# Kernel optimization log

Measured on AMD Instinct MI355X. Metric: run time of the kernel, lower is better.

The kernel has to match this reference:

```python
import jax, jax.numpy as jnp
import numpy as np

N = 50000   # nodes
E = 600000  # edges
F = 128     # num_features
H = 128     # hidden_channels
G = 64      # graphs in batch


def setup_inputs() -> dict:
    key = jax.random.key(0)
    ks = jax.random.split(key, 12)
    x = jax.random.normal(ks[0], (N, F), dtype=jnp.float32)
    edge_index = jax.random.randint(ks[1], (2, E), 0, N, dtype=jnp.int64)
    edge_mask = jax.random.randint(ks[2], (E,), 0, 3, dtype=jnp.int64)
    batch = jnp.sort(jax.random.randint(ks[3], (N,), 0, G, dtype=jnp.int64))
    s = 0.05
    W1 = jax.random.normal(ks[4], (F, H), dtype=jnp.float32) * s
    b1 = jnp.zeros((H,), jnp.float32)
    W2 = jax.random.normal(ks[5], (H, H), dtype=jnp.float32) * s
    b2 = jnp.zeros((H,), jnp.float32)
    W3 = jax.random.normal(ks[6], (H, H), dtype=jnp.float32) * s
    b3 = jnp.zeros((H,), jnp.float32)
    Wl = jax.random.normal(ks[7], (H, 1), dtype=jnp.float32) * s
    bl = jnp.zeros((1,), jnp.float32)
    return {"x": x, "edge_index": edge_index, "edge_mask": edge_mask, "batch": batch,
            "W1": W1, "b1": b1, "W2": W2, "b2": b2, "W3": W3, "b3": b3, "Wl": Wl, "bl": bl}


def gcn_conv(x, W, b, src, dst, ew, n):
    """PyG GCNConv: add self-loops, symmetric deg^-1/2 normalization.
    ew is a {0,1} per-edge weight implementing the dynamic edge subset
    (equivalent to edge_index[:, idx] subsetting, since masked edges
    contribute neither to degree nor to aggregation)."""
    h = x @ W                                                # [n, H]
    deg = jax.ops.segment_sum(ew, dst, num_segments=n) + 1.0  # self-loop adds 1
    dinv = jax.lax.rsqrt(deg)                                # deg^-1/2
    norm = ew * dinv[src] * dinv[dst]                        # per-edge coeff
    agg = jax.ops.segment_sum(h[src] * norm[:, None], dst, num_segments=n)
    agg = agg + h * (dinv * dinv)[:, None]                   # self-loop term 1/deg_i
    return agg + b


def reference(x, edge_index, edge_mask, batch, W1, b1, W2, b2, W3, b3, Wl, bl):
    src, dst = edge_index[0], edge_index[1]
    ones = jnp.ones((E,), x.dtype)
    h = jax.nn.relu(gcn_conv(x, W1, b1, src, dst, ones, N))
    m1 = (edge_mask == 1).astype(x.dtype)
    h = jax.nn.relu(gcn_conv(h, W2, b2, src, dst, m1, N))
    m2 = (edge_mask == 2).astype(x.dtype)
    h = gcn_conv(h, W3, b3, src, dst, m2, N)
    # global_mean_pool over batch ids
    sums = jax.ops.segment_sum(h, batch, num_segments=G)        # [G, H]
    cnt = jax.ops.segment_sum(jnp.ones((N,), h.dtype), batch, num_segments=G)
    pooled = sums / jnp.clip(cnt, 1.0)[:, None]
    # dropout(p=0.3) is identity in eval mode
    return pooled @ Wl + bl
```

## Files before the change

### kernel.cpp

```cpp
#include <hip/hip_runtime.h>

#define NN 50000
#define EE 600000
#define HH 128
#define GG 64
#define NPAD 50176
#define NR 196
#define RN 256
#define NSEC3 150528
#define NRT 588
#define EPB 3072
#define SCAP 3584
#define STAGB 7168

typedef __attribute__((ext_vector_type(8))) short short8;
typedef __attribute__((ext_vector_type(4))) float f32x4;
typedef __attribute__((ext_vector_type(4))) unsigned int u32x4;

__device__ __forceinline__ float bf2f(unsigned int u16) {
    union { unsigned int i; float f; } v; v.i = u16 << 16; return v.f;
}
__device__ __forceinline__ unsigned short f2bf(float f) {
    union { float f; unsigned int i; } v; v.f = f;
    unsigned int u = v.i;
    return (unsigned short)((u + 0x7FFFu + ((u >> 16) & 1u)) >> 16);
}

__device__ __forceinline__ short8 cvt8(f32x4 lo, f32x4 hi) {
    short8 r;
    r[0] = (short)f2bf(lo[0]); r[1] = (short)f2bf(lo[1]);
    r[2] = (short)f2bf(lo[2]); r[3] = (short)f2bf(lo[3]);
    r[4] = (short)f2bf(hi[0]); r[5] = (short)f2bf(hi[1]);
    r[6] = (short)f2bf(hi[2]); r[7] = (short)f2bf(hi[3]);
    return r;
}

__global__ __launch_bounds__(256) void k_part(const int* __restrict__ ei, const int* __restrict__ mask,
                                              int* __restrict__ scnt, unsigned int* __restrict__ sbuf) {
    __shared__ int bcnt[256];
    __shared__ int bcur[256];
    __shared__ int gbase[256];
    int t = threadIdx.x;
    int e0 = blockIdx.x * EPB;
    unsigned int pk[12]; int bin[12];
    bcnt[t] = 0; bcur[t] = 0;
    __syncthreads();
    #pragma unroll
    for (int j = 0; j < 12; j++) {
        int e = e0 + j * 256 + t;
        if (e < EE) {
            int s = ei[e];
            int d = ei[EE + e];
            int m = mask[e];
            pk[j] = (unsigned int)s | ((unsigned int)(d & 255) << 16) | ((unsigned int)m << 24);
            bin[j] = d >> 8;
            atomicAdd(&bcnt[bin[j]], 1);
        } else bin[j] = -1;
    }
    __syncthreads();
    int v = bcnt[t];
    gbase[t] = (v > 0) ? atomicAdd(&scnt[t], v) : 0;
    __syncthreads();
    #pragma unroll
    for (int j = 0; j < 12; j++) {
        if (bin[j] >= 0) {
            int b = bin[j];
            int pos = gbase[b] + atomicAdd(&bcur[b], 1);
            if (pos < SCAP) sbuf[(size_t)b * SCAP + pos] = pk[j];
        }
    }
}

__global__ __launch_bounds__(256) void k_cnt(const int* __restrict__ scnt,
                                             const unsigned int* __restrict__ sbuf,
                                             int* __restrict__ deg, float* __restrict__ dinv,
                                             int* __restrict__ rtot) {
    __shared__ int l0[RN], l1[RN], l2[RN];
    __shared__ int red[12];
    int t = threadIdx.x, lane = t & 63, w = t >> 6;
    int rng = blockIdx.x;
    l0[t] = 0; l1[t] = 0; l2[t] = 0;
    __syncthreads();
    int cnt = scnt[rng]; if (cnt > SCAP) cnt = SCAP;
    const unsigned int* sb = sbuf + (size_t)rng * SCAP;
    for (int i = t; i < cnt; i += 256) {
        unsigned int p = sb[i];
        int dl = (int)((p >> 16) & 255u);
        int m = (int)(p >> 24);
        atomicAdd(&l0[dl], 1);
        if (m == 1) atomicAdd(&l1[dl], 1);
        else if (m == 2) atomicAdd(&l2[dl], 1);
    }
    __syncthreads();
    int node = rng * RN + t;
    int a = l0[t], b = l1[t], c = l2[t];
    deg[node] = a;
    deg[NPAD + node] = b;
    deg[2 * NPAD + node] = c;
    dinv[node] = rsqrtf((float)a + 1.0f);
    dinv[NPAD + node] = rsqrtf((float)b + 1.0f);
    dinv[2 * NPAD + node] = rsqrtf((float)c + 1.0f);
    int sa = a, sb_ = b, sc = c;
    #pragma unroll
    for (int off = 32; off > 0; off >>= 1) {
        sa += __shfl_xor(sa, off); sb_ += __shfl_xor(sb_, off); sc += __shfl_xor(sc, off);
    }
    if (lane == 0) { red[w] = sa; red[4 + w] = sb_; red[8 + w] = sc; }
    __syncthreads();
    if (t == 0) rtot[rng] = red[0] + red[1] + red[2] + red[3];
    else if (t == 1) rtot[NR + rng] = red[4] + red[5] + red[6] + red[7];
    else if (t == 2) rtot[2 * NR + rng] = red[8] + red[9] + red[10] + red[11];
}

__global__ __launch_bounds__(1024) void k_scanR(const int* __restrict__ rtot, int* __restrict__ roff) {
    __shared__ int ws[16];
    int t = threadIdx.x, lane = t & 63, w = t >> 6;
    int v = (t < NRT) ? rtot[t] : 0;
    int x = v;
    #pragma unroll
    for (int off = 1; off < 64; off <<= 1) {
        int u = __shfl_up(x, off);
        if (lane >= off) x += u;
    }
    if (lane == 63) ws[w] = x;
    __syncthreads();
    int wo = 0;
    for (int k = 0; k < w; k++) wo += ws[k];
    if (t < NRT) roff[t] = wo + x - v;
}

__global__ __launch_bounds__(256) void k_build(const int* __restrict__ scnt,
                                               const unsigned int* __restrict__ sbuf,
                                               const int* __restrict__ deg,
                                               const int* __restrict__ roff,
                                               int* __restrict__ rp,
                                               unsigned short* __restrict__ csr) {
    __shared__ int lrp0[RN + 1], lrp1[RN + 1], lrp2[RN + 1];
    __shared__ int lc0[RN], lc1[RN], lc2[RN];
    __shared__ int wsum[12];
    __shared__ unsigned short stag[STAGB];
    int t = threadIdx.x, lane = t & 63, w = t >> 6;
    int rng = blockIdx.x;
    int vd0 = rng * RN;
    int d0 = deg[vd0 + t], d1 = deg[NPAD + vd0 + t], d2 = deg[2 * NPAD + vd0 + t];
    int x0 = d0, x1 = d1, x2 = d2;
    #pragma unroll
    for (int off = 1; off < 64; off <<= 1) {
        int u0 = __shfl_up(x0, off), u1 = __shfl_up(x1, off), u2 = __shfl_up(x2, off);
        if (lane >= off) { x0 += u0; x1 += u1; x2 += u2; }
    }
    if (lane == 63) { wsum[w] = x0; wsum[4 + w] = x1; wsum[8 + w] = x2; }
    __syncthreads();
    int wo0 = 0, wo1 = 0, wo2 = 0;
    for (int k = 0; k < w; k++) { wo0 += wsum[k]; wo1 += wsum[4 + k]; wo2 += wsum[8 + k]; }
    int e0 = wo0 + x0 - d0, e1 = wo1 + x1 - d1, e2 = wo2 + x2 - d2;
    lrp0[t] = e0; lrp1[t] = e1; lrp2[t] = e2;
    if (t == 255) { lrp0[RN] = e0 + d0; lrp1[RN] = e1 + d1; lrp2[RN] = e2 + d2; }
    lc0[t] = 0; lc1[t] = 0; lc2[t] = 0;
    int base0 = roff[rng], base1 = roff[NR + rng], base2 = roff[2 * NR + rng];
    rp[vd0 + t] = base0 + e0;
    rp[NPAD + vd0 + t] = base1 + e1;
    rp[2 * NPAD + vd0 + t] = base2 + e2;
    __syncthreads();
    int c0 = lrp0[RN], c1 = lrp1[RN], c2 = lrp2[RN];
    int cnt = scnt[rng]; if (cnt > SCAP) cnt = SCAP;
    const unsigned int* sb = sbuf + (size_t)rng * SCAP;
    for (int i = t; i < cnt; i += 256) {
        unsigned int p = sb[i];
        unsigned short src = (unsigned short)(p & 0xffffu);
        int dl = (int)((p >> 16) & 255u);
        int m = (int)(p >> 24);
        int sl = lrp0[dl] + atomicAdd(&lc0[dl], 1);
        stag[sl] = src;
        if (m == 1) { sl = c0 + lrp1[dl] + atomicAdd(&lc1[dl], 1); stag[sl] = src; }
        else if (m == 2) { sl = c0 + c1 + lrp2[dl] + atomicAdd(&lc2[dl], 1); stag[sl] = src; }
    }
    __syncthreads();
    for (int i = t; i < c0; i += 256) csr[base0 + i] = stag[i];
    for (int i = t; i < c1; i += 256) csr[base1 + i] = stag[c0 + i];
    for (int i = t; i < c2; i += 256) csr[base2 + i] = stag[c0 + c1 + i];
}

__global__ void k_wt3z(const float* __restrict__ W1, const float* __restrict__ W2,
                       const float* __restrict__ W3, unsigned short* __restrict__ wt,
                       float* __restrict__ sums) {
    int i = blockIdx.x * 256 + threadIdx.x;
    if (i < GG * HH) sums[i] = 0.f;
    int which = i >> 14;
    int r = i & 16383;
    const float* w = (which == 0) ? W1 : (which == 1) ? W2 : W3;
    int k = r >> 7, n = r & 127;
    wt[which * 16384 + n * HH + k] = f2bf(w[r]);
}

__global__ __launch_bounds__(256) void k_gemm_f(const float* __restrict__ in,
                                                const unsigned short* __restrict__ wt,
                                                unsigned short* __restrict__ h) {
    int w = threadIdx.x >> 6, lane = threadIdx.x & 63;
    int lr = lane & 15, lg = lane >> 4;
    int rowbase = (blockIdx.x * 4 + w) * 16;
    if (rowbase >= NN) return;
    int arow = rowbase + lr;
    const f32x4* ap = (const f32x4*)(in + (size_t)arow * HH + lg * 8);
    short8 a0 = cvt8(ap[0], ap[1]);
    short8 a1 = cvt8(ap[8], ap[9]);
    short8 a2 = cvt8(ap[16], ap[17]);
    short8 a3 = cvt8(ap[24], ap[25]);
    f32x4 acc[8];
    #pragma unroll
    for (int i = 0; i < 8; i++) acc[i] = (f32x4){0.f, 0.f, 0.f, 0.f};
    const unsigned short* wbase = wt + lr * HH + lg * 8;
    #pragma unroll
    for (int nc = 0; nc < 8; nc++) {
        const short8* bp = (const short8*)(wbase + nc * 16 * HH);
        short8 b0 = bp[0], b1 = bp[4], b2 = bp[8], b3 = bp[12];
        acc[nc] = __builtin_amdgcn_mfma_f32_16x16x32_bf16(a0, b0, acc[nc], 0, 0, 0);
        acc[nc] = __builtin_amdgcn_mfma_f32_16x16x32_bf16(a1, b1, acc[nc], 0, 0, 0);
        acc[nc] = __builtin_amdgcn_mfma_f32_16x16x32_bf16(a2, b2, acc[nc], 0, 0, 0);
        acc[nc] = __builtin_amdgcn_mfma_f32_16x16x32_bf16(a3, b3, acc[nc], 0, 0, 0);
    }
    int orow = rowbase + lg * 4;
    #pragma unroll
    for (int nc = 0; nc < 8; nc++) {
        #pragma unroll
        for (int j = 0; j < 4; j++) {
            h[(size_t)(orow + j) * HH + nc * 16 + lr] = f2bf(acc[nc][j]);
        }
    }
}

__global__ __launch_bounds__(256) void k_gemm_b(const unsigned short* __restrict__ in,
                                                const unsigned short* __restrict__ wt,
                                                unsigned short* __restrict__ h) {
    int w = threadIdx.x >> 6, lane = threadIdx.x & 63;
    int lr = lane & 15, lg = lane >> 4;
    int rowbase = (blockIdx.x * 4 + w) * 16;
    if (rowbase >= NN) return;
    int arow = rowbase + lr;
    const short8* ap = (const short8*)(in + (size_t)arow * HH + lg * 8);
    short8 a0 = ap[0], a1 = ap[4], a2 = ap[8], a3 = ap[12];
    f32x4 acc[8];
    #pragma unroll
    for (int i = 0; i < 8; i++) acc[i] = (f32x4){0.f, 0.f, 0.f, 0.f};
    const unsigned short* wbase = wt + lr * HH + lg * 8;
    #pragma unroll
    for (int nc = 0; nc < 8; nc++) {
        const short8* bp = (const short8*)(wbase + nc * 16 * HH);
        short8 b0 = bp[0], b1 = bp[4], b2 = bp[8], b3 = bp[12];
        acc[nc] = __builtin_amdgcn_mfma_f32_16x16x32_bf16(a0, b0, acc[nc], 0, 0, 0);
        acc[nc] = __builtin_amdgcn_mfma_f32_16x16x32_bf16(a1, b1, acc[nc], 0, 0, 0);
        acc[nc] = __builtin_amdgcn_mfma_f32_16x16x32_bf16(a2, b2, acc[nc], 0, 0, 0);
        acc[nc] = __builtin_amdgcn_mfma_f32_16x16x32_bf16(a3, b3, acc[nc], 0, 0, 0);
    }
    int orow = rowbase + lg * 4;
    #pragma unroll
    for (int nc = 0; nc < 8; nc++) {
        #pragma unroll
        for (int j = 0; j < 4; j++) {
            h[(size_t)(orow + j) * HH + nc * 16 + lr] = f2bf(acc[nc][j]);
        }
    }
}

__device__ __forceinline__ void agg_edges(const unsigned short* __restrict__ h,
                                          const float* __restrict__ dinv,
                                          const unsigned short* __restrict__ csr,
                                          int e, int end, float di, int l, float* acc) {
    for (; e + 3 < end; e += 4) {
        int s0 = (int)csr[e], s1 = (int)csr[e + 1], s2 = (int)csr[e + 2], s3 = (int)csr[e + 3];
        float w0 = dinv[s0] * di, w1 = dinv[s1] * di, w2 = dinv[s2] * di, w3 = dinv[s3] * di;
        u32x4 v0 = *(const u32x4*)(h + (size_t)s0 * HH + l * 8);
        u32x4 v1 = *(const u32x4*)(h + (size_t)s1 * HH + l * 8);
        u32x4 v2 = *(const u32x4*)(h + (size_t)s2 * HH + l * 8);
        u32x4 v3 = *(const u32x4*)(h + (size_t)s3 * HH + l * 8);
        #pragma unroll
        for (int q = 0; q < 4; q++) {
            acc[2*q]   += w0 * bf2f(v0[q] & 0xffffu); acc[2*q+1] += w0 * bf2f(v0[q] >> 16);
            acc[2*q]   += w1 * bf2f(v1[q] & 0xffffu); acc[2*q+1] += w1 * bf2f(v1[q] >> 16);
            acc[2*q]   += w2 * bf2f(v2[q] & 0xffffu); acc[2*q+1] += w2 * bf2f(v2[q] >> 16);
            acc[2*q]   += w3 * bf2f(v3[q] & 0xffffu); acc[2*q+1] += w3 * bf2f(v3[q] >> 16);
        }
    }
    for (; e < end; e++) {
        int s0 = (int)csr[e];
        float w0 = dinv[s0] * di;
        u32x4 v0 = *(const u32x4*)(h + (size_t)s0 * HH + l * 8);
        #pragma unroll
        for (int q = 0; q < 4; q++) {
            acc[2*q]   += w0 * bf2f(v0[q] & 0xffffu); acc[2*q+1] += w0 * bf2f(v0[q] >> 16);
        }
    }
}

__global__ __launch_bounds__(256) void k_agg(const unsigned short* __restrict__ h,
                                             const float* __restrict__ dinv,
                                             const unsigned short* __restrict__ csr,
                                             const int* __restrict__ rp,
                                             const float* __restrict__ bias,
                                             unsigned short* __restrict__ g) {
    int tid = threadIdx.x;
    int n = blockIdx.x * 16 + (tid >> 4);
    int l = tid & 15;
    float di = dinv[n];
    float c = di * di;
    u32x4 hv = *(const u32x4*)(h + (size_t)n * HH + l * 8);
    float acc[8];
    #pragma unroll
    for (int q = 0; q < 4; q++) {
        acc[2*q] = bf2f(hv[q] & 0xffffu) * c;
        acc[2*q+1] = bf2f(hv[q] >> 16) * c;
    }
    agg_edges(h, dinv, csr, rp[n], rp[n + 1], di, l, acc);
    f32x4 bp0 = *(const f32x4*)(bias + l * 8);
    f32x4 bp1 = *(const f32x4*)(bias + l * 8 + 4);
    acc[0] += bp0[0]; acc[1] += bp0[1]; acc[2] += bp0[2]; acc[3] += bp0[3];
    acc[4] += bp1[0]; acc[5] += bp1[1]; acc[6] += bp1[2]; acc[7] += bp1[3];
    #pragma unroll
    for (int q = 0; q < 8; q++) acc[q] = fmaxf(acc[q], 0.f);
    u32x4 o;
    #pragma unroll
    for (int q = 0; q < 4; q++)
        o[q] = (unsigned int)f2bf(acc[2*q]) | ((unsigned int)f2bf(acc[2*q+1]) << 16);
    *(u32x4*)(g + (size_t)n * HH + l * 8) = o;
}

__global__ __launch_bounds__(256) void k_aggpool(const unsigned short* __restrict__ h,
                                                 const float* __restrict__ dinv,
                                                 const unsigned short* __restrict__ csr,
                                                 const int* __restrict__ rp,
                                                 const float* __restrict__ bias,
                                                 const int* __restrict__ batch,
                                                 float* __restrict__ sums) {
    __shared__ float lsum[4][HH];
    __shared__ int lflag[4];
    int tid = threadIdx.x;
    int n = blockIdx.x * 16 + (tid >> 4);
    int l = tid & 15;
    for (int i = tid; i < 4 * HH; i += 256) ((float*)lsum)[i] = 0.f;
    if (tid < 4) lflag[tid] = 0;
    __syncthreads();
    float di = dinv[n];
    float c = di * di;
    u32x4 hv = *(const u32x4*)(h + (size_t)n * HH + l * 8);
    float acc[8];
    #pragma unroll
    for (int q = 0; q < 4; q++) {
        acc[2*q] = bf2f(hv[q] & 0xffffu) * c;
        acc[2*q+1] = bf2f(hv[q] >> 16) * c;
    }
    agg_edges(h, dinv, csr, rp[n], rp[n + 1], di, l, acc);
    f32x4 bp0 = *(const f32x4*)(bias + l * 8);
    f32x4 bp1 = *(const f32x4*)(bias + l * 8 + 4);
    acc[0] += bp0[0]; acc[1] += bp0[1]; acc[2] += bp0[2]; acc[3] += bp0[3];
    acc[4] += bp1[0]; acc[5] += bp1[1]; acc[6] += bp1[2]; acc[7] += bp1[3];
    int b0 = batch[blockIdx.x * 16];
    int bn = batch[n];
    int rel = bn - b0;
    if (rel < 4) {
        lflag[rel] = 1;
        #pragma unroll
        for (int q = 0; q < 8; q++) atomicAdd(&lsum[rel][l * 8 + q], acc[q]);
    } else {
        #pragma unroll
        for (int q = 0; q < 8; q++) atomicAdd(&sums[bn * HH + l * 8 + q], acc[q]);
    }
    __syncthreads();
    #pragma unroll
    for (int r = 0; r < 4; r++) {
        if (lflag[r]) {
            int gi = b0 + r;
            for (int i = tid; i < HH; i += 256)
                atomicAdd(&sums[gi * HH + i], lsum[r][i]);
        }
    }
}

__device__ __forceinline__ int lbound(const int* a, int n, int key) {
    int lo = 0, hi = n;
    while (lo < hi) { int mid = (lo + hi) >> 1; if (a[mid] < key) lo = mid + 1; else hi = mid; }
    return lo;
}

__global__ __launch_bounds__(128) void k_head(const float* __restrict__ sums,
                                              const int* __restrict__ batch,
                                              const float* __restrict__ Wl,
                                              const float* __restrict__ bl,
                                              float* __restrict__ out) {
    int gid = blockIdx.x;
    int t = threadIdx.x;
    int lo = lbound(batch, NN, gid);
    int hi = lbound(batch, NN, gid + 1);
    float cnt = (float)(hi - lo);
    if (cnt < 1.f) cnt = 1.f;
    float prod = (sums[gid * HH + t] / cnt) * Wl[t];
    __shared__ float sm[128];
    sm[t] = prod;
    __syncthreads();
    for (int off = 64; off > 0; off >>= 1) {
        if (t < off) sm[t] += sm[t + off];
        __syncthreads();
    }
    if (t == 0) out[gid] = sm[0] + bl[0];
}

extern "C" void kernel_launch(void* const* d_in, const int* in_sizes, int n_in,
                              void* d_out, int out_size, void* d_ws, size_t ws_size,
                              hipStream_t stream) {
    const float* x    = (const float*)d_in[0];
    const int*   ei   = (const int*)d_in[1];
    const int*   mask = (const int*)d_in[2];
    const int*   batch= (const int*)d_in[3];
    const float* W1   = (const float*)d_in[4];
    const float* b1   = (const float*)d_in[5];
    const float* W2   = (const float*)d_in[6];
    const float* b2   = (const float*)d_in[7];
    const float* W3   = (const float*)d_in[8];
    const float* b3   = (const float*)d_in[9];
    const float* Wl   = (const float*)d_in[10];
    const float* bl   = (const float*)d_in[11];
    float* out = (float*)d_out;

    char* ws = (char*)d_ws;
    unsigned short* g = (unsigned short*)(ws + 0);
    unsigned short* h = (unsigned short*)(ws + 12800000);
    unsigned short* wt1 = (unsigned short*)(ws + 25600000);
    unsigned short* wt2 = wt1 + 16384;
    unsigned short* wt3 = wt2 + 16384;
    int* deg   = (int*)(ws + 25698304);
    float* dinv= (float*)(ws + 26300416);
    int* rp    = (int*)(ws + 26902528);
    int* rtot  = (int*)(ws + 27505152);
    int* roff  = (int*)(ws + 27509248);
    int* scnt  = (int*)(ws + 27513344);
    unsigned short* csr = (unsigned short*)(ws + 27514368);
    unsigned int* sbuf = (unsigned int*)(ws + 29914368);
    float* sums = (float*)(ws + 32724224);

    float* dinv1 = dinv;
    float* dinv2 = dinv + NPAD;
    float* dinv3 = dinv + 2 * NPAD;

    hipMemsetAsync(scnt, 0, (size_t)NR * sizeof(int), stream);

    dim3 b256(256);
    k_part<<<dim3((EE + EPB - 1) / EPB), b256, 0, stream>>>(ei, mask, scnt, sbuf);
    k_cnt<<<dim3(NR), b256, 0, stream>>>(scnt, sbuf, deg, dinv, rtot);
    k_scanR<<<dim3(1), dim3(1024), 0, stream>>>(rtot, roff);
    k_build<<<dim3(NR), b256, 0, stream>>>(scnt, sbuf, deg, roff, rp, csr);

    k_wt3z<<<dim3(192), b256, 0, stream>>>(W1, W2, W3, wt1, sums);

    dim3 ggrid((NN + 63) / 64);
    dim3 agrid(NN / 16);

    k_gemm_f<<<ggrid, b256, 0, stream>>>(x, wt1, h);
    k_agg<<<agrid, b256, 0, stream>>>(h, dinv1, csr, rp, b1, g);
    k_gemm_b<<<ggrid, b256, 0, stream>>>(g, wt2, h);
    k_agg<<<agrid, b256, 0, stream>>>(h, dinv2, csr, rp + NPAD, b2, g);
    k_gemm_b<<<ggrid, b256, 0, stream>>>(g, wt3, h);
    k_aggpool<<<agrid, b256, 0, stream>>>(h, dinv3, csr, rp + 2 * NPAD, b3, batch, sums);

    k_head<<<dim3(GG), dim3(128), 0, stream>>>(sums, batch, Wl, bl, out);
}
```

Measured before the change: 198.0 us.

## Pre-scale GEMM outputs by source dinv and simplify aggregation, split pooling

The GEMM epilogues now multiply each output row by its own deg^-1/2, so the aggregation becomes a plain sum of neighbor rows scaled once by the destination dinv. This removes the per-edge gather of dinv and the per-edge multiply. The aggregation loop is unrolled by 8, and the fused aggregate-plus-pool kernel is replaced by a plain aggregate followed by a separate segmented pooling kernel. The memset of the counters is folded into the weight-conversion kernel, which now launches first. In exchange, the final layer writes its output to memory and the pooling kernel reads it back. Rounding also shifts slightly because the dinv scaling is applied before the bf16 conversion.

```diff
diff --git a/kernel.cpp b/kernel.cpp
--- a/kernel.cpp
+++ b/kernel.cpp
@@ -33,6 +33,19 @@
     r[4] = (short)f2bf(hi[0]); r[5] = (short)f2bf(hi[1]);
     r[6] = (short)f2bf(hi[2]); r[7] = (short)f2bf(hi[3]);
     return r;
+}
+
+__global__ void k_wt3z(const float* __restrict__ W1, const float* __restrict__ W2,
+                       const float* __restrict__ W3, unsigned short* __restrict__ wt,
+                       float* __restrict__ sums, int* __restrict__ scnt) {
+    int i = blockIdx.x * 256 + threadIdx.x;
+    if (i < GG * HH) sums[i] = 0.f;
+    if (i < NR) scnt[i] = 0;
+    int which = i >> 14;
+    int r = i & 16383;
+    const float* w = (which == 0) ? W1 : (which == 1) ? W2 : W3;
+    int k = r >> 7, n = r & 127;
+    wt[which * 16384 + n * HH + k] = f2bf(w[r]);
 }
 
 __global__ __launch_bounds__(256) void k_part(const int* __restrict__ ei, const int* __restrict__ mask,
@@ -181,20 +194,9 @@
     for (int i = t; i < c2; i += 256) csr[base2 + i] = stag[c0 + c1 + i];
 }
 
-__global__ void k_wt3z(const float* __restrict__ W1, const float* __restrict__ W2,
-                       const float* __restrict__ W3, unsigned short* __restrict__ wt,
-                       float* __restrict__ sums) {
-    int i = blockIdx.x * 256 + threadIdx.x;
-    if (i < GG * HH) sums[i] = 0.f;
-    int which = i >> 14;
-    int r = i & 16383;
-    const float* w = (which == 0) ? W1 : (which == 1) ? W2 : W3;
-    int k = r >> 7, n = r & 127;
-    wt[which * 16384 + n * HH + k] = f2bf(w[r]);
-}
-
 __global__ __launch_bounds__(256) void k_gemm_f(const float* __restrict__ in,
                                                 const unsigned short* __restrict__ wt,
+                                                const float* __restrict__ dinv,
                                                 unsigned short* __restrict__ h) {
     int w = threadIdx.x >> 6, lane = threadIdx.x & 63;
     int lr = lane & 15, lg = lane >> 4;
@@ -220,17 +222,19 @@
         acc[nc] = __builtin_amdgcn_mfma_f32_16x16x32_bf16(a3, b3, acc[nc], 0, 0, 0);
     }
     int orow = rowbase + lg * 4;
+    f32x4 dv = *(const f32x4*)(dinv + orow);
     #pragma unroll
     for (int nc = 0; nc < 8; nc++) {
         #pragma unroll
         for (int j = 0; j < 4; j++) {
-            h[(size_t)(orow + j) * HH + nc * 16 + lr] = f2bf(acc[nc][j]);
+            h[(size_t)(orow + j) * HH + nc * 16 + lr] = f2bf(acc[nc][j] * dv[j]);
         }
     }
 }
 
 __global__ __launch_bounds__(256) void k_gemm_b(const unsigned short* __restrict__ in,
                                                 const unsigned short* __restrict__ wt,
+                                                const float* __restrict__ dinv,
                                                 unsigned short* __restrict__ h) {
     int w = threadIdx.x >> 6, lane = threadIdx.x & 63;
     int lr = lane & 15, lg = lane >> 4;
@@ -253,70 +257,88 @@
         acc[nc] = __builtin_amdgcn_mfma_f32_16x16x32_bf16(a3, b3, acc[nc], 0, 0, 0);
     }
     int orow = rowbase + lg * 4;
+    f32x4 dv = *(const f32x4*)(dinv + orow);
     #pragma unroll
     for (int nc = 0; nc < 8; nc++) {
         #pragma unroll
         for (int j = 0; j < 4; j++) {
-            h[(size_t)(orow + j) * HH + nc * 16 + lr] = f2bf(acc[nc][j]);
-        }
-    }
-}
-
-__device__ __forceinline__ void agg_edges(const unsigned short* __restrict__ h,
-                                          const float* __restrict__ dinv,
-                                          const unsigned short* __restrict__ csr,
-                                          int e, int end, float di, int l, float* acc) {
+            h[(size_t)(orow + j) * HH + nc * 16 + lr] = f2bf(acc[nc][j] * dv[j]);
+        }
+    }
+}
+
+__global__ __launch_bounds__(256) void k_agg(const unsigned short* __restrict__ h,
+                                             const float* __restrict__ dinv,
+                                             const unsigned short* __restrict__ csr,
+                                             const int* __restrict__ rp,
+                                             const float* __restrict__ bias,
+                                             unsigned short* __restrict__ g,
+                                             int relu) {
+    int tid = threadIdx.x;
+    int n = blockIdx.x * 16 + (tid >> 4);
+    int l = tid & 15;
+    u32x4 hv = *(const u32x4*)(h + (size_t)n * HH + l * 8);
+    float acc[8];
+    #pragma unroll
+    for (int q = 0; q < 4; q++) {
+        acc[2*q] = bf2f(hv[q] & 0xffffu);
+        acc[2*q+1] = bf2f(hv[q] >> 16);
+    }
+    int e = rp[n], end = rp[n + 1];
+    for (; e + 7 < end; e += 8) {
+        int s0 = (int)csr[e],     s1 = (int)csr[e + 1], s2 = (int)csr[e + 2], s3 = (int)csr[e + 3];
+        int s4 = (int)csr[e + 4], s5 = (int)csr[e + 5], s6 = (int)csr[e + 6], s7 = (int)csr[e + 7];
+        u32x4 v0 = *(const u32x4*)(h + (size_t)s0 * HH + l * 8);
+        u32x4 v1 = *(const u32x4*)(h + (size_t)s1 * HH + l * 8);
+        u32x4 v2 = *(const u32x4*)(h + (size_t)s2 * HH + l * 8);
+        u32x4 v3 = *(const u32x4*)(h + (size_t)s3 * HH + l * 8);
+        u32x4 v4 = *(const u32x4*)(h + (size_t)s4 * HH + l * 8);
+        u32x4 v5 = *(const u32x4*)(h + (size_t)s5 * HH + l * 8);
+        u32x4 v6 = *(const u32x4*)(h + (size_t)s6 * HH + l * 8);
+        u32x4 v7 = *(const u32x4*)(h + (size_t)s7 * HH + l * 8);
+        #pragma unroll
+        for (int q = 0; q < 4; q++) {
+            acc[2*q] += bf2f(v0[q] & 0xffffu); acc[2*q+1] += bf2f(v0[q] >> 16);
+            acc[2*q] += bf2f(v1[q] & 0xffffu); acc[2*q+1] += bf2f(v1[q] >> 16);
+            acc[2*q] += bf2f(v2[q] & 0xffffu); acc[2*q+1] += bf2f(v2[q] >> 16);
+            acc[2*q] += bf2f(v3[q] & 0xffffu); acc[2*q+1] += bf2f(v3[q] >> 16);
+            acc[2*q] += bf2f(v4[q] & 0xffffu); acc[2*q+1] += bf2f(v4[q] >> 16);
+            acc[2*q] += bf2f(v5[q] & 0xffffu); acc[2*q+1] += bf2f(v5[q] >> 16);
+            acc[2*q] += bf2f(v6[q] & 0xffffu); acc[2*q+1] += bf2f(v6[q] >> 16);
+            acc[2*q] += bf2f(v7[q] & 0xffffu); acc[2*q+1] += bf2f(v7[q] >> 16);
+        }
+    }
     for (; e + 3 < end; e += 4) {
         int s0 = (int)csr[e], s1 = (int)csr[e + 1], s2 = (int)csr[e + 2], s3 = (int)csr[e + 3];
-        float w0 = dinv[s0] * di, w1 = dinv[s1] * di, w2 = dinv[s2] * di, w3 = dinv[s3] * di;
         u32x4 v0 = *(const u32x4*)(h + (size_t)s0 * HH + l * 8);
         u32x4 v1 = *(const u32x4*)(h + (size_t)s1 * HH + l * 8);
         u32x4 v2 = *(const u32x4*)(h + (size_t)s2 * HH + l * 8);
         u32x4 v3 = *(const u32x4*)(h + (size_t)s3 * HH + l * 8);
         #pragma unroll
         for (int q = 0; q < 4; q++) {
-            acc[2*q]   += w0 * bf2f(v0[q] & 0xffffu); acc[2*q+1] += w0 * bf2f(v0[q] >> 16);
-            acc[2*q]   += w1 * bf2f(v1[q] & 0xffffu); acc[2*q+1] += w1 * bf2f(v1[q] >> 16);
-            acc[2*q]   += w2 * bf2f(v2[q] & 0xffffu); acc[2*q+1] += w2 * bf2f(v2[q] >> 16);
-            acc[2*q]   += w3 * bf2f(v3[q] & 0xffffu); acc[2*q+1] += w3 * bf2f(v3[q] >> 16);
+            acc[2*q] += bf2f(v0[q] & 0xffffu); acc[2*q+1] += bf2f(v0[q] >> 16);
+            acc[2*q] += bf2f(v1[q] & 0xffffu); acc[2*q+1] += bf2f(v1[q] >> 16);
+            acc[2*q] += bf2f(v2[q] & 0xffffu); acc[2*q+1] += bf2f(v2[q] >> 16);
+            acc[2*q] += bf2f(v3[q] & 0xffffu); acc[2*q+1] += bf2f(v3[q] >> 16);
         }
     }
     for (; e < end; e++) {
         int s0 = (int)csr[e];
-        float w0 = dinv[s0] * di;
         u32x4 v0 = *(const u32x4*)(h + (size_t)s0 * HH + l * 8);
         #pragma unroll
         for (int q = 0; q < 4; q++) {
-            acc[2*q]   += w0 * bf2f(v0[q] & 0xffffu); acc[2*q+1] += w0 * bf2f(v0[q] >> 16);
-        }
-    }
-}
-
-__global__ __launch_bounds__(256) void k_agg(const unsigned short* __restrict__ h,
-                                             const float* __restrict__ dinv,
-                                             const unsigned short* __restrict__ csr,
-                                             const int* __restrict__ rp,
-                                             const float* __restrict__ bias,
-                                             unsigned short* __restrict__ g) {
-    int tid = threadIdx.x;
-    int n = blockIdx.x * 16 + (tid >> 4);
-    int l = tid & 15;
+            acc[2*q] += bf2f(v0[q] & 0xffffu); acc[2*q+1] += bf2f(v0[q] >> 16);
+        }
+    }
     float di = dinv[n];
-    float c = di * di;
-    u32x4 hv = *(const u32x4*)(h + (size_t)n * HH + l * 8);
-    float acc[8];
-    #pragma unroll
-    for (int q = 0; q < 4; q++) {
-        acc[2*q] = bf2f(hv[q] & 0xffffu) * c;
-        acc[2*q+1] = bf2f(hv[q] >> 16) * c;
-    }
-    agg_edges(h, dinv, csr, rp[n], rp[n + 1], di, l, acc);
     f32x4 bp0 = *(const f32x4*)(bias + l * 8);
     f32x4 bp1 = *(const f32x4*)(bias + l * 8 + 4);
-    acc[0] += bp0[0]; acc[1] += bp0[1]; acc[2] += bp0[2]; acc[3] += bp0[3];
-    acc[4] += bp1[0]; acc[5] += bp1[1]; acc[6] += bp1[2]; acc[7] += bp1[3];
-    #pragma unroll
-    for (int q = 0; q < 8; q++) acc[q] = fmaxf(acc[q], 0.f);
+    float bb[8] = {bp0[0], bp0[1], bp0[2], bp0[3], bp1[0], bp1[1], bp1[2], bp1[3]};
+    #pragma unroll
+    for (int q = 0; q < 8; q++) {
+        acc[q] = acc[q] * di + bb[q];
+        if (relu) acc[q] = fmaxf(acc[q], 0.f);
+    }
     u32x4 o;
     #pragma unroll
     for (int q = 0; q < 4; q++)
@@ -324,55 +346,24 @@
     *(u32x4*)(g + (size_t)n * HH + l * 8) = o;
 }
 
-__global__ __launch_bounds__(256) void k_aggpool(const unsigned short* __restrict__ h,
-                                                 const float* __restrict__ dinv,
-                                                 const unsigned short* __restrict__ csr,
-                                                 const int* __restrict__ rp,
-                                                 const float* __restrict__ bias,
-                                                 const int* __restrict__ batch,
-                                                 float* __restrict__ sums) {
-    __shared__ float lsum[4][HH];
-    __shared__ int lflag[4];
-    int tid = threadIdx.x;
-    int n = blockIdx.x * 16 + (tid >> 4);
-    int l = tid & 15;
-    for (int i = tid; i < 4 * HH; i += 256) ((float*)lsum)[i] = 0.f;
-    if (tid < 4) lflag[tid] = 0;
-    __syncthreads();
-    float di = dinv[n];
-    float c = di * di;
-    u32x4 hv = *(const u32x4*)(h + (size_t)n * HH + l * 8);
-    float acc[8];
-    #pragma unroll
-    for (int q = 0; q < 4; q++) {
-        acc[2*q] = bf2f(hv[q] & 0xffffu) * c;
-        acc[2*q+1] = bf2f(hv[q] >> 16) * c;
-    }
-    agg_edges(h, dinv, csr, rp[n], rp[n + 1], di, l, acc);
-    f32x4 bp0 = *(const f32x4*)(bias + l * 8);
-    f32x4 bp1 = *(const f32x4*)(bias + l * 8 + 4);
-    acc[0] += bp0[0]; acc[1] += bp0[1]; acc[2] += bp0[2]; acc[3] += bp0[3];
-    acc[4] += bp1[0]; acc[5] += bp1[1]; acc[6] += bp1[2]; acc[7] += bp1[3];
-    int b0 = batch[blockIdx.x * 16];
-    int bn = batch[n];
-    int rel = bn - b0;
-    if (rel < 4) {
-        lflag[rel] = 1;
-        #pragma unroll
-        for (int q = 0; q < 8; q++) atomicAdd(&lsum[rel][l * 8 + q], acc[q]);
-    } else {
-        #pragma unroll
-        for (int q = 0; q < 8; q++) atomicAdd(&sums[bn * HH + l * 8 + q], acc[q]);
-    }
-    __syncthreads();
-    #pragma unroll
-    for (int r = 0; r < 4; r++) {
-        if (lflag[r]) {
-            int gi = b0 + r;
-            for (int i = tid; i < HH; i += 256)
-                atomicAdd(&sums[gi * HH + i], lsum[r][i]);
-        }
-    }
+__global__ __launch_bounds__(128) void k_pool_part(const unsigned short* __restrict__ g3,
+                                                   const int* __restrict__ batch,
+                                                   float* __restrict__ sums) {
+    int t = threadIdx.x;
+    int n0 = blockIdx.x * 64;
+    int n1 = n0 + 64; if (n1 > NN) n1 = NN;
+    int curb = batch[n0];
+    float acc = 0.f;
+    for (int n = n0; n < n1; n++) {
+        int b = batch[n];
+        if (b != curb) {
+            atomicAdd(&sums[curb * HH + t], acc);
+            acc = 0.f;
+            curb = b;
+        }
+        acc += bf2f((unsigned int)g3[(size_t)n * HH + t]);
+    }
+    atomicAdd(&sums[curb * HH + t], acc);
 }
 
 __device__ __forceinline__ int lbound(const int* a, int n, int key) {
@@ -440,25 +431,23 @@
     float* dinv2 = dinv + NPAD;
     float* dinv3 = dinv + 2 * NPAD;
 
-    hipMemsetAsync(scnt, 0, (size_t)NR * sizeof(int), stream);
-
     dim3 b256(256);
+    k_wt3z<<<dim3(192), b256, 0, stream>>>(W1, W2, W3, wt1, sums, scnt);
     k_part<<<dim3((EE + EPB - 1) / EPB), b256, 0, stream>>>(ei, mask, scnt, sbuf);
     k_cnt<<<dim3(NR), b256, 0, stream>>>(scnt, sbuf, deg, dinv, rtot);
     k_scanR<<<dim3(1), dim3(1024), 0, stream>>>(rtot, roff);
     k_build<<<dim3(NR), b256, 0, stream>>>(scnt, sbuf, deg, roff, rp, csr);
 
-    k_wt3z<<<dim3(192), b256, 0, stream>>>(W1, W2, W3, wt1, sums);
-
     dim3 ggrid((NN + 63) / 64);
     dim3 agrid(NN / 16);
 
-    k_gemm_f<<<ggrid, b256, 0, stream>>>(x, wt1, h);
-    k_agg<<<agrid, b256, 0, stream>>>(h, dinv1, csr, rp, b1, g);
-    k_gemm_b<<<ggrid, b256, 0, stream>>>(g, wt2, h);
-    k_agg<<<agrid, b256, 0, stream>>>(h, dinv2, csr, rp + NPAD, b2, g);
-    k_gemm_b<<<ggrid, b256, 0, stream>>>(g, wt3, h);
-    k_aggpool<<<agrid, b256, 0, stream>>>(h, dinv3, csr, rp + 2 * NPAD, b3, batch, sums);
-
+    k_gemm_f<<<ggrid, b256, 0, stream>>>(x, wt1, dinv1, h);
+    k_agg<<<agrid, b256, 0, stream>>>(h, dinv1, csr, rp, b1, g, 1);
+    k_gemm_b<<<ggrid, b256, 0, stream>>>(g, wt2, dinv2, h);
+    k_agg<<<agrid, b256, 0, stream>>>(h, dinv2, csr, rp + NPAD, b2, g, 1);
+    k_gemm_b<<<ggrid, b256, 0, stream>>>(g, wt3, dinv3, h);
+    k_agg<<<agrid, b256, 0, stream>>>(h, dinv3, csr, rp + 2 * NPAD, b3, g, 0);
+
+    k_pool_part<<<dim3((NN + 63) / 64), dim3(128), 0, stream>>>(g, batch, sums);
     k_head<<<dim3(GG), dim3(128), 0, stream>>>(sums, batch, Wl, bl, out);
 }
```

Measured after the change: 187.4 us. 1.06x faster.
